# Performance work log

Measured on AMD Instinct MI355X. Metric: run time of the kernel, lower is better.

## Reference

```python
import jax, jax.numpy as jnp
import numpy as np

B, HIDDEN, NH, MAX_S = 8, 4096, 32, 4096
HD = HIDDEN // NH  # 128
POS = 2047  # current cache write position (tokens 0..POS-1 already cached)


def setup_inputs() -> dict:
    key = jax.random.key(0)
    ks = jax.random.split(key, 7)
    x = jax.random.normal(ks[0], (B, 1, HIDDEN), dtype=jnp.float32)
    cached_k = jax.random.normal(ks[1], (B, NH, MAX_S, HD), dtype=jnp.float32)
    cached_v = jax.random.normal(ks[2], (B, NH, MAX_S, HD), dtype=jnp.float32)
    scale = 0.02
    wq = jax.random.normal(ks[3], (HIDDEN, HIDDEN), dtype=jnp.float32) * scale
    wk = jax.random.normal(ks[4], (HIDDEN, HIDDEN), dtype=jnp.float32) * scale
    wv = jax.random.normal(ks[5], (HIDDEN, HIDDEN), dtype=jnp.float32) * scale
    wo = jax.random.normal(ks[6], (HIDDEN, HIDDEN), dtype=jnp.float32) * scale
    return {"x": x, "cached_k": cached_k, "cached_v": cached_v,
            "wq": wq, "wk": wk, "wv": wv, "wo": wo, "cached_pos": POS}


def reference(x, cached_k, cached_v, wq, wk, wv, wo, cached_pos):
    # Decode step: seq_len == 1 (is_training=False path of the torch module).
    b, s, hidden = x.shape  # s == 1
    # Projections (torch Linear: y = x @ W.T), reshape to [B, H, 1, D]
    q = (x @ wq.T).reshape(b, s, NH, HD).transpose(0, 2, 1, 3)
    k = (x @ wk.T).reshape(b, s, NH, HD).transpose(0, 2, 1, 3)
    v = (x @ wv.T).reshape(b, s, NH, HD).transpose(0, 2, 1, 3)
    # Append new token's K/V into the cache at cached_pos (static python int)
    ck = cached_k.at[:, :, cached_pos, :].set(k[:, :, 0, :])
    cv = cached_v.at[:, :, cached_pos, :].set(v[:, :, 0, :])
    # Attend over the valid prefix [0, cached_pos]
    kk = ck[:, :, :cached_pos + 1, :]  # [B, H, T, D]
    vv = cv[:, :, :cached_pos + 1, :]
    scores = jnp.einsum('bhqd,bhkd->bhqk', q, kk) / jnp.sqrt(jnp.float32(HD))
    att = jax.nn.softmax(scores, axis=-1)  # stable softmax == module's _softmax
    out = jnp.einsum('bhqk,bhkd->bhqd', att, vv)  # [B, H, 1, D]
    out = out.transpose(0, 2, 1, 3).reshape(b, s, hidden)
    return out @ wo.T
```

## Files before the change

kernel.cpp:

```cpp
#include <hip/hip_runtime.h>
#include <cmath>

#define B_     8
#define NH_    32
#define HD_    128
#define HID_   4096
#define MAXS_  4096
#define NPAIR_ (B_ * NH_)
#define NEG_BIG_ (-1e30f)

typedef float f4_ __attribute__((ext_vector_type(4)));

__device__ __forceinline__ f4_ ntload4(const float* p) {
  return __builtin_nontemporal_load((const f4_*)p);
}
__device__ __forceinline__ f4_ ld4(const float* p) {
  return *(const f4_*)p;
}
__device__ __forceinline__ float dot4(f4_ a, f4_ b) {
  f4_ m = a * b;
  return m.x + m.y + m.z + m.w;
}

template<int NSL>
__global__ __launch_bounds__(64) void gemv8p(
    const float* __restrict__ W0, const float* __restrict__ W1,
    const float* __restrict__ W2, const float* __restrict__ x,
    float* __restrict__ out, int nb_per_mat, int n_inner, int part_stride)
{
  const int bid   = blockIdx.x;
  const int ks    = bid / n_inner;
  const int inner = bid % n_inner;
  const int m     = inner / nb_per_mat;
  const int r0    = (inner % nb_per_mat) * 8;
  const float* __restrict__ W = (m == 0) ? W0 : ((m == 1) ? W1 : W2);
  float* o = out + (size_t)ks * part_stride + m * (B_ * HID_);

  const int lane = threadIdx.x;
  const int kofs = ks * NSL * 256;

  float acc[8][8];
#pragma unroll
  for (int r = 0; r < 8; ++r)
#pragma unroll
    for (int b = 0; b < 8; ++b) acc[r][b] = 0.f;

  const float* Wp = W + (size_t)r0 * HID_ + kofs + lane * 4;
  const float* xp = x + kofs + lane * 4;

  f4_ wa[8], wb[8], xa[8], xb[8];
#pragma unroll
  for (int r = 0; r < 8; ++r) wa[r] = ld4(Wp + (size_t)r * HID_);
#pragma unroll
  for (int b = 0; b < 8; ++b) xa[b] = ld4(xp + b * HID_);

#pragma unroll 1
  for (int u = 0; u < NSL; u += 2) {
    {
      const int j1 = (u + 1) * 256;
#pragma unroll
      for (int r = 0; r < 8; ++r) wb[r] = ld4(Wp + (size_t)r * HID_ + j1);
#pragma unroll
      for (int b = 0; b < 8; ++b) xb[b] = ld4(xp + b * HID_ + j1);
#pragma unroll
      for (int r = 0; r < 8; ++r)
#pragma unroll
        for (int b = 0; b < 8; ++b) acc[r][b] += dot4(wa[r], xa[b]);
    }
    {
      if (u + 2 < NSL) {
        const int j2 = (u + 2) * 256;
#pragma unroll
        for (int r = 0; r < 8; ++r) wa[r] = ld4(Wp + (size_t)r * HID_ + j2);
#pragma unroll
        for (int b = 0; b < 8; ++b) xa[b] = ld4(xp + b * HID_ + j2);
      }
#pragma unroll
      for (int r = 0; r < 8; ++r)
#pragma unroll
        for (int b = 0; b < 8; ++b) acc[r][b] += dot4(wb[r], xb[b]);
    }
  }

#pragma unroll
  for (int r = 0; r < 8; ++r)
#pragma unroll
    for (int b = 0; b < 8; ++b) {
      float v = acc[r][b];
#pragma unroll
      for (int off = 32; off; off >>= 1) v += __shfl_xor(v, off);
      acc[r][b] = v;
    }

  if (lane == 0) {
#pragma unroll
    for (int r = 0; r < 8; ++r)
#pragma unroll
      for (int b = 0; b < 8; ++b)
        o[(size_t)b * HID_ + r0 + r] = acc[r][b];
  }
}

__global__ __launch_bounds__(256) void sum4(
    const float* __restrict__ part, float* __restrict__ out)
{
  const int gid = blockIdx.x * 256 + threadIdx.x;
  const int i = gid * 4;
  f4_ v = ld4(part + i) + ld4(part + (B_ * HID_) + i)
        + ld4(part + 2 * (B_ * HID_) + i) + ld4(part + 3 * (B_ * HID_) + i);
  *(f4_*)(out + i) = v;
}

__global__ __launch_bounds__(512) void attn_pair(
    const float* __restrict__ qkv, const float* __restrict__ ck,
    const float* __restrict__ cv, const int* __restrict__ ppos,
    float* __restrict__ attnout)
{
  __shared__ float sm[8], sl[8];
  __shared__ float sacc[8][HD_];

  const int pos  = *ppos;
  const int pair = blockIdx.x;
  const int b    = pair >> 5;
  const int h    = pair & (NH_ - 1);
  const int w    = threadIdx.x >> 6;
  const int lane = threadIdx.x & 63;
  const int half = lane >> 5, l32 = lane & 31;
  const int k0   = w * 256;

  float m = NEG_BIG_, l = 0.f;
  f4_ acc = (f4_)0.f;

  if (k0 <= pos) {
    const float scale = 0.08838834764831845f;
    const int hoff = b * HID_ + h * HD_ + l32 * 4;
    f4_ q4  = ld4(qkv + hoff) * scale;
    f4_ kf4 = ld4(qkv + B_ * HID_ + hoff);
    f4_ vf4 = ld4(qkv + 2 * B_ * HID_ + hoff);
    const float* ckh = ck + ((size_t)(b * NH_ + h)) * MAXS_ * HD_;
    const float* cvh = cv + ((size_t)(b * NH_ + h)) * MAXS_ * HD_;

    for (int c = 0; c < 16; ++c) {
      const int kbase = k0 + c * 16;
      f4_ k4[8], v4[8];
#pragma unroll
      for (int j = 0; j < 8; ++j) {
        const int ki = kbase + 2 * j + half;
        k4[j] = ntload4(ckh + (size_t)ki * HD_ + l32 * 4);
        v4[j] = ntload4(cvh + (size_t)ki * HD_ + l32 * 4);
      }
#pragma unroll
      for (int j = 0; j < 8; ++j) {
        const int ki = kbase + 2 * j + half;
        if (ki == pos) { k4[j] = kf4; v4[j] = vf4; }
      }

      float sc[8];
#pragma unroll
      for (int j = 0; j < 8; ++j) sc[j] = dot4(q4, k4[j]);

#pragma unroll
      for (int off = 16; off >= 1; off >>= 1)
#pragma unroll
        for (int j = 0; j < 8; ++j) sc[j] += __shfl_xor(sc[j], off);

#pragma unroll
      for (int j = 0; j < 8; ++j) {
        const int ki = kbase + 2 * j + half;
        if (ki > pos) sc[j] = -INFINITY;
      }

      const float cm = fmaxf(fmaxf(fmaxf(sc[0], sc[1]), fmaxf(sc[2], sc[3])),
                             fmaxf(fmaxf(sc[4], sc[5]), fmaxf(sc[6], sc[7])));
      const float mn   = fmaxf(m, cm);
      const float corr = __expf(m - mn);
      float p[8], ps = 0.f;
#pragma unroll
      for (int j = 0; j < 8; ++j) { p[j] = __expf(sc[j] - mn); ps += p[j]; }
      l = l * corr + ps;
      acc *= corr;
#pragma unroll
      for (int j = 0; j < 8; ++j) acc += p[j] * v4[j];
      m = mn;
    }
  }

  const float mo = __shfl_xor(m, 32);
  const float lo = __shfl_xor(l, 32);
  f4_ ao;
  ao.x = __shfl_xor(acc.x, 32); ao.y = __shfl_xor(acc.y, 32);
  ao.z = __shfl_xor(acc.z, 32); ao.w = __shfl_xor(acc.w, 32);
  const float mm = fmaxf(m, mo);
  const float w0 = __expf(m - mm), w1 = __expf(mo - mm);
  const float lm = l * w0 + lo * w1;
  f4_ am = acc * w0 + ao * w1;

  if (half == 0) {
    *(f4_*)&sacc[w][l32 * 4] = am;
    if (l32 == 0) { sm[w] = mm; sl[w] = lm; }
  }
  __syncthreads();

  if (threadIdx.x < 32) {
    const int t = threadIdx.x;
    float mg = NEG_BIG_;
#pragma unroll
    for (int u = 0; u < 8; ++u)
      if (sl[u] > 0.f) mg = fmaxf(mg, sm[u]);
    float ls = 0.f;
    f4_ o = (f4_)0.f;
#pragma unroll
    for (int u = 0; u < 8; ++u)
      if (sl[u] > 0.f) {
        const float wu = __expf(sm[u] - mg);
        ls += sl[u] * wu;
        o  += wu * ld4(&sacc[u][t * 4]);
      }
    *(f4_*)(attnout + pair * HD_ + t * 4) = o / ls;
  }
}

extern "C" void kernel_launch(void* const* d_in, const int* in_sizes, int n_in,
                              void* d_out, int out_size, void* d_ws, size_t ws_size,
                              hipStream_t stream) {
  const float* x  = (const float*)d_in[0];
  const float* ck = (const float*)d_in[1];
  const float* cv = (const float*)d_in[2];
  const float* wq = (const float*)d_in[3];
  const float* wk = (const float*)d_in[4];
  const float* wv = (const float*)d_in[5];
  const float* wo = (const float*)d_in[6];
  const int* pos  = (const int*)d_in[7];
  float* out = (float*)d_out;
  float* ws  = (float*)d_ws;

  float* qkv     = ws;
  float* attnout = qkv + 3 * B_ * HID_;
  float* wopart  = attnout + B_ * HID_;

  gemv8p<16><<<3 * 512, 64, 0, stream>>>(wq, wk, wv, x, qkv,
                                         512, 3 * 512, 0);
  attn_pair<<<NPAIR_, 512, 0, stream>>>(qkv, ck, cv, pos, attnout);
  gemv8p<4><<<4 * 512, 64, 0, stream>>>(wo, wo, wo, attnout, wopart,
                                        512, 512, B_ * HID_);
  sum4<<<(B_ * HID_) / (256 * 4), 256, 0, stream>>>(wopart, out);
}
```

Measured before the change: 176.4 us.

## Stage activation vector in LDS and share it across four-wave GEMV blocks

The GEMV kernel now runs four waves per block, each handling 8 rows, for 32 rows per block. The x activations for the block's K slice are copied once into LDS with global_load_lds instead of every wave reloading them from global memory. The QKV projection is also split into two K-partitions whose partial sums the attention kernel adds together. This cuts redundant x traffic and changes the grid shape, at the cost of a large dynamic LDS allocation (64 KB) that may limit occupancy.

```diff
diff --git a/kernel.cpp b/kernel.cpp
--- a/kernel.cpp
+++ b/kernel.cpp
@@ -1,5 +1,6 @@
 #include <hip/hip_runtime.h>
 #include <cmath>
+#include <cstdint>
 
 #define B_     8
 #define NH_    32
@@ -7,6 +8,7 @@
 #define HID_   4096
 #define MAXS_  4096
 #define NPAIR_ (B_ * NH_)
+#define QS_    (3 * B_ * HID_)
 #define NEG_BIG_ (-1e30f)
 
 typedef float f4_ __attribute__((ext_vector_type(4)));
@@ -22,22 +24,32 @@
   return m.x + m.y + m.z + m.w;
 }
 
+__device__ __forceinline__ void stage16(const float* gsrc, unsigned ldsoff) {
+  __builtin_amdgcn_global_load_lds(
+      (__attribute__((address_space(1))) void*)(uintptr_t)gsrc,
+      (__attribute__((address_space(3))) void*)ldsoff,
+      16, 0, 0);
+}
+
 template<int NSL>
-__global__ __launch_bounds__(64) void gemv8p(
+__global__ __launch_bounds__(256) void gemv_xlds(
     const float* __restrict__ W0, const float* __restrict__ W1,
     const float* __restrict__ W2, const float* __restrict__ x,
     float* __restrict__ out, int nb_per_mat, int n_inner, int part_stride)
 {
+  extern __shared__ float dyn[];
   const int bid   = blockIdx.x;
   const int ks    = bid / n_inner;
   const int inner = bid % n_inner;
   const int m     = inner / nb_per_mat;
-  const int r0    = (inner % nb_per_mat) * 8;
+  const int r0    = (inner % nb_per_mat) * 32;
   const float* __restrict__ W = (m == 0) ? W0 : ((m == 1) ? W1 : W2);
   float* o = out + (size_t)ks * part_stride + m * (B_ * HID_);
 
-  const int lane = threadIdx.x;
+  const int wib  = threadIdx.x >> 6;
+  const int lane = threadIdx.x & 63;
   const int kofs = ks * NSL * 256;
+  const int rw   = r0 + wib * 8;
 
   float acc[8][8];
 #pragma unroll
@@ -45,42 +57,53 @@
 #pragma unroll
     for (int b = 0; b < 8; ++b) acc[r][b] = 0.f;
 
-  const float* Wp = W + (size_t)r0 * HID_ + kofs + lane * 4;
+  const float* Wp = W + (size_t)rw * HID_ + kofs + lane * 4;
   const float* xp = x + kofs + lane * 4;
 
-  f4_ wa[8], wb[8], xa[8], xb[8];
+#pragma unroll
+  for (int bb = 0; bb < 2; ++bb) {
+    const int b = 2 * wib + bb;
+#pragma unroll
+    for (int s = 0; s < NSL; ++s)
+      stage16(xp + (size_t)b * HID_ + s * 256,
+              (unsigned)((b * NSL + s) * 1024));
+  }
+
+  f4_ wa[8], wb[8];
 #pragma unroll
   for (int r = 0; r < 8; ++r) wa[r] = ld4(Wp + (size_t)r * HID_);
-#pragma unroll
-  for (int b = 0; b < 8; ++b) xa[b] = ld4(xp + b * HID_);
+  __syncthreads();
+
+#define COMP_(BUF, u)                                                         \
+  {                                                                           \
+    f4_ xv[8];                                                                \
+    _Pragma("unroll")                                                         \
+    for (int b = 0; b < 8; ++b)                                               \
+      xv[b] = ld4(&dyn[(b * NSL + (u)) * 256 + lane * 4]);                    \
+    _Pragma("unroll")                                                         \
+    for (int r = 0; r < 8; ++r)                                               \
+      _Pragma("unroll")                                                       \
+      for (int b = 0; b < 8; ++b) acc[r][b] += dot4(BUF[r], xv[b]);           \
+  }
 
 #pragma unroll 1
   for (int u = 0; u < NSL; u += 2) {
     {
-      const int j1 = (u + 1) * 256;
-#pragma unroll
-      for (int r = 0; r < 8; ++r) wb[r] = ld4(Wp + (size_t)r * HID_ + j1);
-#pragma unroll
-      for (int b = 0; b < 8; ++b) xb[b] = ld4(xp + b * HID_ + j1);
 #pragma unroll
       for (int r = 0; r < 8; ++r)
-#pragma unroll
-        for (int b = 0; b < 8; ++b) acc[r][b] += dot4(wa[r], xa[b]);
+        wb[r] = ld4(Wp + (size_t)r * HID_ + (u + 1) * 256);
+      COMP_(wa, u);
     }
     {
       if (u + 2 < NSL) {
-        const int j2 = (u + 2) * 256;
-#pragma unroll
-        for (int r = 0; r < 8; ++r) wa[r] = ld4(Wp + (size_t)r * HID_ + j2);
-#pragma unroll
-        for (int b = 0; b < 8; ++b) xa[b] = ld4(xp + b * HID_ + j2);
-      }
-#pragma unroll
-      for (int r = 0; r < 8; ++r)
-#pragma unroll
-        for (int b = 0; b < 8; ++b) acc[r][b] += dot4(wb[r], xb[b]);
-    }
-  }
+#pragma unroll
+        for (int r = 0; r < 8; ++r)
+          wa[r] = ld4(Wp + (size_t)r * HID_ + (u + 2) * 256);
+      }
+      COMP_(wb, u + 1);
+    }
+  }
+#undef COMP_
 
 #pragma unroll
   for (int r = 0; r < 8; ++r)
@@ -97,7 +120,7 @@
     for (int r = 0; r < 8; ++r)
 #pragma unroll
       for (int b = 0; b < 8; ++b)
-        o[(size_t)b * HID_ + r0 + r] = acc[r][b];
+        o[(size_t)b * HID_ + rw + r] = acc[r][b];
   }
 }
 
@@ -134,9 +157,9 @@
   if (k0 <= pos) {
     const float scale = 0.08838834764831845f;
     const int hoff = b * HID_ + h * HD_ + l32 * 4;
-    f4_ q4  = ld4(qkv + hoff) * scale;
-    f4_ kf4 = ld4(qkv + B_ * HID_ + hoff);
-    f4_ vf4 = ld4(qkv + 2 * B_ * HID_ + hoff);
+    f4_ q4  = (ld4(qkv + hoff) + ld4(qkv + QS_ + hoff)) * scale;
+    f4_ kf4 =  ld4(qkv + B_ * HID_ + hoff) + ld4(qkv + QS_ + B_ * HID_ + hoff);
+    f4_ vf4 =  ld4(qkv + 2 * B_ * HID_ + hoff) + ld4(qkv + QS_ + 2 * B_ * HID_ + hoff);
     const float* ckh = ck + ((size_t)(b * NH_ + h)) * MAXS_ * HD_;
     const float* cvh = cv + ((size_t)(b * NH_ + h)) * MAXS_ * HD_;
 
@@ -234,14 +257,14 @@
   float* out = (float*)d_out;
   float* ws  = (float*)d_ws;
 
-  float* qkv     = ws;
-  float* attnout = qkv + 3 * B_ * HID_;
+  float* qkvp    = ws;
+  float* attnout = qkvp + 2 * QS_;
   float* wopart  = attnout + B_ * HID_;
 
-  gemv8p<16><<<3 * 512, 64, 0, stream>>>(wq, wk, wv, x, qkv,
-                                         512, 3 * 512, 0);
-  attn_pair<<<NPAIR_, 512, 0, stream>>>(qkv, ck, cv, pos, attnout);
-  gemv8p<4><<<4 * 512, 64, 0, stream>>>(wo, wo, wo, attnout, wopart,
-                                        512, 512, B_ * HID_);
+  gemv_xlds<8><<<2 * 3 * 128, 256, 65536, stream>>>(wq, wk, wv, x, qkvp,
+                                                    128, 3 * 128, QS_);
+  attn_pair<<<NPAIR_, 512, 0, stream>>>(qkvp, ck, cv, pos, attnout);
+  gemv_xlds<4><<<4 * 128, 256, 32768, stream>>>(wo, wo, wo, attnout, wopart,
+                                                128, 128, B_ * HID_);
   sum4<<<(B_ * HID_) / (256 * 4), 256, 0, stream>>>(wopart, out);
 }
```

Result: faster. 163.1 us, median of 2 (-7.6%).
